# Optimization experiments

Hardware: AMD Instinct MI355X
Metric: run time of the kernel (lower is better)

## Reference

```python
import jax, jax.numpy as jnp
import numpy as np

EPS = 1e-5
C = 64  # in_channels == feat_channels == out_channels


def _ln(x, g, b):
    m = jnp.mean(x, axis=-1, keepdims=True)
    v = jnp.mean(jnp.square(x - m), axis=-1, keepdims=True)
    return (x - m) * jax.lax.rsqrt(v + EPS) * g + b


def setup_inputs() -> dict:
    key = jax.random.key(0)
    ks = jax.random.split(key, 10)
    bs, nc, H, W = 8, 80, 256, 256
    d = {
        "feat": jax.random.normal(ks[0], (bs, C, H, W), jnp.float32),
        "head": jax.random.normal(ks[1], (bs, nc, C, 1), jnp.float32),
        "pred": jax.random.normal(ks[2], (bs, nc, H // 2, W // 2), jnp.float32),
        # linear transforms (stored [in, out], applied as x @ W + b)
        "W_pred_t": jax.random.normal(ks[3], (C, 2 * C), jnp.float32) * 0.05,
        "b_pred_t": jnp.zeros((2 * C,), jnp.float32),
        "W_head_t": jax.random.normal(ks[4], (C, 2 * C), jnp.float32) * 0.05,
        "b_head_t": jnp.zeros((2 * C,), jnp.float32),
        "W_pred_g": jax.random.normal(ks[5], (C, C), jnp.float32) * 0.05,
        "b_pred_g": jnp.zeros((C,), jnp.float32),
        "W_head_g": jax.random.normal(ks[6], (C, C), jnp.float32) * 0.05,
        "b_head_g": jnp.zeros((C,), jnp.float32),
        "W_fc": jax.random.normal(ks[7], (C, C), jnp.float32) * 0.05,
        "b_fc": jnp.zeros((C,), jnp.float32),
        # layernorm params
        "g_pin": jnp.ones((C,), jnp.float32), "be_pin": jnp.zeros((C,), jnp.float32),
        "g_hin": jnp.ones((C,), jnp.float32), "be_hin": jnp.zeros((C,), jnp.float32),
        "g_pout": jnp.ones((C,), jnp.float32), "be_pout": jnp.zeros((C,), jnp.float32),
        "g_hout": jnp.ones((C,), jnp.float32), "be_hout": jnp.zeros((C,), jnp.float32),
        "g_fc": jnp.ones((C,), jnp.float32), "be_fc": jnp.zeros((C,), jnp.float32),
    }
    return d


def reference(feat, head, pred,
              W_pred_t, b_pred_t, W_head_t, b_head_t,
              W_pred_g, b_pred_g, W_head_g, b_head_g,
              W_fc, b_fc,
              g_pin, be_pin, g_hin, be_hin,
              g_pout, be_pout, g_hout, be_hout,
              g_fc, be_fc):
    bs, nc = head.shape[:2]
    H, W = feat.shape[2], feat.shape[3]
    pred_up = jax.image.resize(pred, (bs, nc, H, W), method="bilinear")
    pred_up = jax.nn.sigmoid(pred_up)
    # head-aware feature assembly: [bs, nc, C]
    assemble = jnp.einsum("bnhw,bchw->bnc", pred_up, feat)
    a = assemble.reshape(-1, C)                      # [BN, C]
    BN = a.shape[0]
    # head: [bs, nc, C, kk] -> [BN, kk, C]
    hd = jnp.transpose(head.reshape(bs, nc, C, -1), (0, 1, 3, 2)).reshape(BN, -1, C)

    pf = a @ W_pred_t + b_pred_t                     # [BN, 2C]
    pf_in, pf_out = pf[:, :C], pf[:, C:]
    hf = hd @ W_head_t + b_head_t                    # [BN, kk, 2C]
    hf_in, hf_out = hf[..., :C], hf[..., C:]

    gate = hf_in * pf_in[:, None, :]                 # [BN, kk, C]
    head_gate = jax.nn.sigmoid(_ln(gate @ W_head_g + b_head_g, g_hin, be_hin))
    pred_gate = jax.nn.sigmoid(_ln(gate @ W_pred_g + b_pred_g, g_pin, be_pin))

    hf_out = _ln(hf_out, g_hout, be_hout)
    pf_out = _ln(pf_out, g_pout, be_pout)

    upd = pred_gate * pf_out[:, None, :] + head_gate * hf_out
    upd = jax.nn.relu(_ln(upd @ W_fc + b_fc, g_fc, be_fc))
    upd = upd.reshape(bs, nc, -1, C)
    upd = jnp.transpose(upd, (0, 1, 3, 2)).reshape(bs, nc, C, 1, 1)
    return upd
```

## Files before the change

### kernel.cpp

```cpp
#include <hip/hip_runtime.h>
#include <hip/hip_bf16.h>
#include <hip/hip_fp16.h>


using bf16x8 = __attribute__((ext_vector_type(8))) short;
using f32x4  = __attribute__((ext_vector_type(4))) float;

#define SCHED_FENCE() __builtin_amdgcn_sched_barrier(0)
#define LGKM_BARRIER() do { \
  asm volatile("s_waitcnt lgkmcnt(0)" ::: "memory"); \
  __builtin_amdgcn_s_barrier(); } while (0)
#define GLD4(dst, ptr) \
  asm volatile("global_load_dwordx4 %0, %1, off" : "=v"(dst) : "v"(ptr) : "memory")
#define GLD1(dst, ptr) \
  asm volatile("global_load_dword %0, %1, off" : "=v"(dst) : "v"(ptr) : "memory")
#define WAITV(n) do { \
  asm volatile("s_waitcnt vmcnt(" #n ")" ::: "memory"); \
  __builtin_amdgcn_sched_barrier(0); } while (0)

__device__ __forceinline__ unsigned pk2(float lo, float hi) {
  union { __hip_bfloat162 h2; unsigned u; } cv;
  cv.h2 = __float22bfloat162_rn(make_float2(lo, hi));
  return cv.u;
}
__device__ __forceinline__ float sigAB(float a, float b) {
  return __builtin_amdgcn_rcpf(1.0f + __builtin_amdgcn_exp2f(-0.36067376f * a - 1.08202128f * b));
}
__device__ __forceinline__ float sigBA(float a, float b) {
  return __builtin_amdgcn_rcpf(1.0f + __builtin_amdgcn_exp2f(-1.08202128f * a - 0.36067376f * b));
}

__global__ __launch_bounds__(256, 3) void k_assemble_half(
    const float* __restrict__ feat, const float* __restrict__ pred,
    __half* __restrict__ partial) {
  __shared__ __align__(16) unsigned short Pfrag[20 * 64 * 8];

  const int bid = blockIdx.x;
  const int wg  = (bid & 7) * 512 + (bid >> 3);
  const int half = wg & 1;
  const int h    = (wg >> 1) & 255;
  const int b    = wg >> 9;

  const int tid = threadIdx.x;
  const int gg = tid & 15, nbp = tid >> 4;
  const int wid = tid >> 6, l = tid & 63;
  const int ch16 = l & 15, kg = l >> 4, c0 = wid << 4;

  const int j = h >> 1;
  int r0, r1; float wy0, wy1;
  if ((h & 1) == 0) { r0 = (j > 0) ? j - 1 : 0; r1 = j; wy0 = 0.25f; wy1 = 0.75f; }
  else              { r0 = j; r1 = (j < 127) ? j + 1 : 127; wy0 = 0.75f; wy1 = 0.25f; }

  const int cbase = half << 6;
  const int csc   = 64 - half;
  const float* pbat = pred + (((size_t)(b * 80)) << 14);

  f32x4 p0[5], p1[5];
  float s0[5], s1[5];
  f32x4 f[8];
  #pragma unroll
  for (int i = 0; i < 5; ++i) {
    const float* pb = pbat + (((size_t)(nbp + 16 * i)) << 14);
    GLD4(p0[i], pb + (r0 << 7) + cbase + 4 * gg);
    GLD4(p1[i], pb + (r1 << 7) + cbase + 4 * gg);
  }
  #pragma unroll
  for (int i = 0; i < 5; ++i) {
    const float* pb = pbat + (((size_t)(nbp + 16 * i)) << 14);
    GLD1(s0[i], pb + (r0 << 7) + csc);
    GLD1(s1[i], pb + (r1 << 7) + csc);
  }
  const float* fb = feat + (((size_t)(b * 64 + c0 + ch16)) << 16) + h * 256 + (half << 7);
  #pragma unroll
  for (int ks = 0; ks < 4; ++ks) {
    GLD4(f[2 * ks],     fb + ks * 32 + kg * 8);
    GLD4(f[2 * ks + 1], fb + ks * 32 + kg * 8 + 4);
  }

  WAITV(8);

  #pragma unroll
  for (int i = 0; i < 5; ++i) {
    const float sc = wy0 * s0[i] + wy1 * s1[i];
    const float y0 = wy0 * p0[i][0] + wy1 * p1[i][0];
    const float y1 = wy0 * p0[i][1] + wy1 * p1[i][1];
    const float y2 = wy0 * p0[i][2] + wy1 * p1[i][2];
    const float y3 = wy0 * p0[i][3] + wy1 * p1[i][3];
    float yl = __shfl_up(y3, 1, 16);
    float yr = __shfl_down(y0, 1, 16);
    if (gg == 0)  yl = half ? sc : y0;
    if (gg == 15) yr = half ? y3 : sc;
    float P[8];
    P[0] = sigAB(yl, y0); P[1] = sigBA(y0, y1);
    P[2] = sigAB(y0, y1); P[3] = sigBA(y1, y2);
    P[4] = sigAB(y1, y2); P[5] = sigBA(y2, y3);
    P[6] = sigAB(y2, y3); P[7] = sigBA(y3, yr);
    uint4 s;
    s.x = pk2(P[0], P[1]); s.y = pk2(P[2], P[3]);
    s.z = pk2(P[4], P[5]); s.w = pk2(P[6], P[7]);
    const int ks = gg >> 2, kgw = gg & 3;
    const int slot = kgw * 16 + ((nbp ^ ks ^ (kgw << 1)) & 15);
    *(uint4*)&Pfrag[(((ks * 5 + i) * 64) + slot) * 8] = s;
  }
  LGKM_BARRIER();

  f32x4 acc[5] = {};
  #pragma unroll
  for (int ks = 0; ks < 4; ++ks) {
    if (ks == 0)      WAITV(6);
    else if (ks == 1) WAITV(4);
    else if (ks == 2) WAITV(2);
    else              WAITV(0);
    const f32x4 f0 = f[2 * ks], f1 = f[2 * ks + 1];
    union { uint4 u; bf16x8 v; } bu;
    bu.u.x = pk2(f0[0], f0[1]); bu.u.y = pk2(f0[2], f0[3]);
    bu.u.z = pk2(f1[0], f1[1]); bu.u.w = pk2(f1[2], f1[3]);
    const int slot = kg * 16 + ((ch16 ^ ks ^ (kg << 1)) & 15);
    #pragma unroll
    for (int m = 0; m < 5; ++m) {
      const bf16x8 af = *(const bf16x8*)&Pfrag[(((ks * 5 + m) * 64) + slot) * 8];
      acc[m] = __builtin_amdgcn_mfma_f32_16x16x32_bf16(af, bu.v, acc[m], 0, 0, 0);
    }
  }

  __half* po = partial + ((size_t)(b * 512 + h * 2 + half)) * (80 * 64);
  #pragma unroll
  for (int m = 0; m < 5; ++m) {
    #pragma unroll
    for (int q = 0; q < 4; ++q) {
      const int n = m * 16 + kg * 4 + q;
      po[n * 64 + c0 + ch16] = __float2half(acc[m][q]);
    }
  }
}

__global__ __launch_bounds__(256) void k_assemble_full(
    const float* __restrict__ feat, const float* __restrict__ pred,
    __half* __restrict__ partial) {
  __shared__ __align__(16) unsigned short Pfrag[40 * 64 * 8];

  const int tid = threadIdx.x;
  const int b  = blockIdx.x >> 7;
  const int rb = blockIdx.x & 127;
  const int wid = tid >> 6, l = tid & 63;
  const int ch16 = l & 15, kg = l >> 4;
  const int c0 = wid << 4;
  const int h0 = rb * 2;
  const int gg = tid & 31, nb = tid >> 5;

  f32x4 acc[5] = {};
  const float* fwave = feat + (((size_t)(b * 64 + c0 + ch16)) << 16);
  const float* pbat  = pred + (((size_t)(b * 80)) << 14);

  #pragma unroll
  for (int r = 0; r < 2; ++r) {
    const int h = h0 + r;
    const int j = h >> 1;
    int r0, r1; float wy0, wy1;
    if ((h & 1) == 0) { r0 = (j > 0) ? j - 1 : 0; r1 = j; wy0 = 0.25f; wy1 = 0.75f; }
    else              { r0 = j; r1 = (j < 127) ? j + 1 : 127; wy0 = 0.75f; wy1 = 0.25f; }

    float4 p0[10], p1[10];
    #pragma unroll
    for (int i = 0; i < 10; ++i) {
      const float* pb = pbat + (((size_t)(nb + 8 * i)) << 14);
      p0[i] = *(const float4*)(pb + (r0 << 7) + gg * 4);
      p1[i] = *(const float4*)(pb + (r1 << 7) + gg * 4);
    }
    SCHED_FENCE();

    const float* fb = fwave + h * 256;
    float4 f[16];
    #pragma unroll
    for (int ks = 0; ks < 8; ++ks) {
      const int pw = ks * 32 + kg * 8;
      f[2 * ks]     = *(const float4*)(fb + pw);
      f[2 * ks + 1] = *(const float4*)(fb + pw + 4);
    }
    SCHED_FENCE();

    #pragma unroll
    for (int i = 0; i < 10; ++i) {
      const int n = nb + 8 * i;
      const float y0 = wy0 * p0[i].x + wy1 * p1[i].x;
      const float y1 = wy0 * p0[i].y + wy1 * p1[i].y;
      const float y2 = wy0 * p0[i].z + wy1 * p1[i].z;
      const float y3 = wy0 * p0[i].w + wy1 * p1[i].w;
      float yl = __shfl_up(y3, 1, 64);   if (gg == 0)  yl = y0;
      float yr = __shfl_down(y0, 1, 64); if (gg == 31) yr = y3;
      float P[8];
      P[0] = sigAB(yl, y0); P[1] = sigBA(y0, y1);
      P[2] = sigAB(y0, y1); P[3] = sigBA(y1, y2);
      P[4] = sigAB(y1, y2); P[5] = sigBA(y2, y3);
      P[6] = sigAB(y2, y3); P[7] = sigBA(y3, yr);
      uint4 s;
      s.x = pk2(P[0], P[1]); s.y = pk2(P[2], P[3]);
      s.z = pk2(P[4], P[5]); s.w = pk2(P[6], P[7]);
      const int ks = gg >> 2, kgw = gg & 3;
      const int slot = kgw * 16 + (((n & 15) ^ ks ^ (kgw << 1)) & 15);
      *(uint4*)&Pfrag[(((ks * 5 + (n >> 4)) * 64) + slot) * 8] = s;
    }
    LGKM_BARRIER();

    #pragma unroll
    for (int ks = 0; ks < 8; ++ks) {
      const float4 f0 = f[2 * ks], f1 = f[2 * ks + 1];
      union { uint4 u; bf16x8 v; } bu;
      bu.u.x = pk2(f0.x, f0.y); bu.u.y = pk2(f0.z, f0.w);
      bu.u.z = pk2(f1.x, f1.y); bu.u.w = pk2(f1.z, f1.w);
      const int slot = kg * 16 + ((ch16 ^ ks ^ (kg << 1)) & 15);
      #pragma unroll
      for (int m = 0; m < 5; ++m) {
        const bf16x8 af = *(const bf16x8*)&Pfrag[(((ks * 5 + m) * 64) + slot) * 8];
        acc[m] = __builtin_amdgcn_mfma_f32_16x16x32_bf16(af, bu.v, acc[m], 0, 0, 0);
      }
    }
    LGKM_BARRIER();
  }

  __half* po = partial + ((size_t)(b * 128 + rb)) * (80 * 64);
  #pragma unroll
  for (int m = 0; m < 5; ++m) {
    #pragma unroll
    for (int q = 0; q < 4; ++q) {
      const int n = m * 16 + kg * 4 + q;
      po[n * 64 + c0 + ch16] = __float2half(acc[m][q]);
    }
  }
}

__device__ __forceinline__ float wred64(float v) {
  #pragma unroll
  for (int off = 32; off > 0; off >>= 1) v += __shfl_xor(v, off, 64);
  return v;
}
__device__ __forceinline__ float lnorm(float x, const float* __restrict__ g,
                                       const float* __restrict__ be, int l) {
  const float m = wred64(x) * 0.015625f;
  const float d = x - m;
  const float var = wred64(d * d) * 0.015625f;
  return d * rsqrtf(var + 1e-5f) * g[l] + be[l];
}
__device__ __forceinline__ float sigmf(float x) {
  return __builtin_amdgcn_rcpf(1.0f + __builtin_amdgcn_exp2f(-1.44269504f * x));
}

__global__ __launch_bounds__(256) void k_head(
    const __half* __restrict__ partial, const float* __restrict__ head,
    const float* __restrict__ Wpt, const float* __restrict__ bpt,
    const float* __restrict__ Wht, const float* __restrict__ bht,
    const float* __restrict__ Wpg, const float* __restrict__ bpg,
    const float* __restrict__ Whg, const float* __restrict__ bhg,
    const float* __restrict__ Wfc, const float* __restrict__ bfc,
    const float* __restrict__ g_pin, const float* __restrict__ be_pin,
    const float* __restrict__ g_hin, const float* __restrict__ be_hin,
    const float* __restrict__ g_pout, const float* __restrict__ be_pout,
    const float* __restrict__ g_hout, const float* __restrict__ be_hout,
    const float* __restrict__ g_fc, const float* __restrict__ be_fc,
    float* __restrict__ out, int npart) {
  __shared__ float red[4][64];
  __shared__ float buf[4][64];
  const int tid = threadIdx.x, c = tid & 63, q = tid >> 6;
  const int r = blockIdx.x;
  const int b = r / 80, n = r % 80;
  const int npq = npart >> 2;

  const __half* pp = partial + ((size_t)b * npart + (size_t)q * npq) * 5120 + n * 64 + c;
  float s = 0.f;
  #pragma unroll 8
  for (int jj = 0; jj < npq; ++jj) s += __half2float(pp[(size_t)jj * 5120]);
  red[q][c] = s;
  __syncthreads();

  if (q == 0) {
    const float a_c = red[0][c] + red[1][c] + red[2][c] + red[3][c];
    buf[0][c] = a_c;
    buf[1][c] = head[(size_t)r * 64 + c];

    float pf_in = bpt[c], pf_out = bpt[64 + c];
    float hf_in = bht[c], hf_out = bht[64 + c];
    #pragma unroll 8
    for (int k = 0; k < 64; ++k) {
      const float av = buf[0][k];
      const float hv = buf[1][k];
      pf_in  += av * Wpt[k * 128 + c];
      pf_out += av * Wpt[k * 128 + 64 + c];
      hf_in  += hv * Wht[k * 128 + c];
      hf_out += hv * Wht[k * 128 + 64 + c];
    }
    buf[2][c] = hf_in * pf_in;

    float hg = bhg[c], pg = bpg[c];
    #pragma unroll 8
    for (int k = 0; k < 64; ++k) {
      const float gv = buf[2][k];
      hg += gv * Whg[k * 64 + c];
      pg += gv * Wpg[k * 64 + c];
    }
    const float head_gate = sigmf(lnorm(hg, g_hin, be_hin, c));
    const float pred_gate = sigmf(lnorm(pg, g_pin, be_pin, c));
    const float hfo = lnorm(hf_out, g_hout, be_hout, c);
    const float pfo = lnorm(pf_out, g_pout, be_pout, c);
    buf[3][c] = pred_gate * pfo + head_gate * hfo;

    float fc = bfc[c];
    #pragma unroll 8
    for (int k = 0; k < 64; ++k)
      fc += buf[3][k] * Wfc[k * 64 + c];
    float o = lnorm(fc, g_fc, be_fc, c);
    out[(size_t)r * 64 + c] = fmaxf(o, 0.f);
  }
}

extern "C" void kernel_launch(void* const* d_in, const int* in_sizes, int n_in,
                              void* d_out, int out_size, void* d_ws, size_t ws_size,
                              hipStream_t stream) {
  const float* feat   = (const float*)d_in[0];
  const float* head   = (const float*)d_in[1];
  const float* pred   = (const float*)d_in[2];
  const float* Wpt    = (const float*)d_in[3];
  const float* bpt    = (const float*)d_in[4];
  const float* Wht    = (const float*)d_in[5];
  const float* bht    = (const float*)d_in[6];
  const float* Wpg    = (const float*)d_in[7];
  const float* bpg    = (const float*)d_in[8];
  const float* Whg    = (const float*)d_in[9];
  const float* bhg    = (const float*)d_in[10];
  const float* Wfc    = (const float*)d_in[11];
  const float* bfc    = (const float*)d_in[12];
  const float* g_pin  = (const float*)d_in[13];
  const float* be_pin = (const float*)d_in[14];
  const float* g_hin  = (const float*)d_in[15];
  const float* be_hin = (const float*)d_in[16];
  const float* g_pout = (const float*)d_in[17];
  const float* be_pout= (const float*)d_in[18];
  const float* g_hout = (const float*)d_in[19];
  const float* be_hout= (const float*)d_in[20];
  const float* g_fc   = (const float*)d_in[21];
  const float* be_fc  = (const float*)d_in[22];
  float* out = (float*)d_out;
  __half* partial = (__half*)d_ws;

  const bool big = ws_size >= (size_t)8 * 512 * 5120 * 2;
  const int npart = big ? 512 : 128;

  if (big)
    hipLaunchKernelGGL(k_assemble_half, dim3(4096), dim3(256), 0, stream,
                       feat, pred, partial);
  else
    hipLaunchKernelGGL(k_assemble_full, dim3(1024), dim3(256), 0, stream,
                       feat, pred, partial);

  hipLaunchKernelGGL(k_head, dim3(640), dim3(256), 0, stream,
                     partial, head, Wpt, bpt, Wht, bht, Wpg, bpg, Whg, bhg,
                     Wfc, bfc, g_pin, be_pin, g_hin, be_hin, g_pout, be_pout,
                     g_hout, be_hout, g_fc, be_fc, out, npart);
}
```

Measured before the change: 61.28 us.

## Load feat tiles directly into LDS via global_load_lds instead of registers

```diff
diff --git a/kernel.cpp b/kernel.cpp
--- a/kernel.cpp
+++ b/kernel.cpp
@@ -10,13 +10,6 @@
 #define LGKM_BARRIER() do { \
   asm volatile("s_waitcnt lgkmcnt(0)" ::: "memory"); \
   __builtin_amdgcn_s_barrier(); } while (0)
-#define GLD4(dst, ptr) \
-  asm volatile("global_load_dwordx4 %0, %1, off" : "=v"(dst) : "v"(ptr) : "memory")
-#define GLD1(dst, ptr) \
-  asm volatile("global_load_dword %0, %1, off" : "=v"(dst) : "v"(ptr) : "memory")
-#define WAITV(n) do { \
-  asm volatile("s_waitcnt vmcnt(" #n ")" ::: "memory"); \
-  __builtin_amdgcn_sched_barrier(0); } while (0)
 
 __device__ __forceinline__ unsigned pk2(float lo, float hi) {
   union { __hip_bfloat162 h2; unsigned u; } cv;
@@ -30,9 +23,10 @@
   return __builtin_amdgcn_rcpf(1.0f + __builtin_amdgcn_exp2f(-1.08202128f * a - 0.36067376f * b));
 }
 
-__global__ __launch_bounds__(256, 3) void k_assemble_half(
+__global__ __launch_bounds__(256) void k_assemble_half(
     const float* __restrict__ feat, const float* __restrict__ pred,
     __half* __restrict__ partial) {
+  __shared__ __align__(16) float FeatLds[4][2048];
   __shared__ __align__(16) unsigned short Pfrag[20 * 64 * 8];
 
   const int bid = blockIdx.x;
@@ -57,27 +51,31 @@
 
   f32x4 p0[5], p1[5];
   float s0[5], s1[5];
-  f32x4 f[8];
   #pragma unroll
   for (int i = 0; i < 5; ++i) {
     const float* pb = pbat + (((size_t)(nbp + 16 * i)) << 14);
-    GLD4(p0[i], pb + (r0 << 7) + cbase + 4 * gg);
-    GLD4(p1[i], pb + (r1 << 7) + cbase + 4 * gg);
-  }
-  #pragma unroll
-  for (int i = 0; i < 5; ++i) {
-    const float* pb = pbat + (((size_t)(nbp + 16 * i)) << 14);
-    GLD1(s0[i], pb + (r0 << 7) + csc);
-    GLD1(s1[i], pb + (r1 << 7) + csc);
-  }
-  const float* fb = feat + (((size_t)(b * 64 + c0 + ch16)) << 16) + h * 256 + (half << 7);
-  #pragma unroll
-  for (int ks = 0; ks < 4; ++ks) {
-    GLD4(f[2 * ks],     fb + ks * 32 + kg * 8);
-    GLD4(f[2 * ks + 1], fb + ks * 32 + kg * 8 + 4);
-  }
-
-  WAITV(8);
+    p0[i] = *(const f32x4*)(pb + (r0 << 7) + cbase + 4 * gg);
+    p1[i] = *(const f32x4*)(pb + (r1 << 7) + cbase + 4 * gg);
+    s0[i] = pb[(r0 << 7) + csc];
+    s1[i] = pb[(r1 << 7) + csc];
+  }
+  SCHED_FENCE();
+
+  {
+    const float* fbase = feat + (((size_t)(b * 64 + c0)) << 16) + h * 256 + (half << 7);
+    const int kg_r = l >> 4, y = l & 15;
+    #pragma unroll
+    for (int i = 0; i < 8; ++i) {
+      const int ks = i >> 1, h2 = i & 1;
+      const int ch_r = (y ^ ks ^ (kg_r << 1)) & 15;
+      const float* src = fbase + (((size_t)ch_r) << 16) + ks * 32 + kg_r * 8 + h2 * 4;
+      __builtin_amdgcn_global_load_lds(
+          (const __attribute__((address_space(1))) void*)src,
+          (__attribute__((address_space(3))) void*)((char*)&FeatLds[wid][0] + i * 1024),
+          16, 0, 0);
+    }
+  }
+  SCHED_FENCE();
 
   #pragma unroll
   for (int i = 0; i < 5; ++i) {
@@ -102,20 +100,18 @@
     const int slot = kgw * 16 + ((nbp ^ ks ^ (kgw << 1)) & 15);
     *(uint4*)&Pfrag[(((ks * 5 + i) * 64) + slot) * 8] = s;
   }
-  LGKM_BARRIER();
+  __syncthreads();
 
   f32x4 acc[5] = {};
+  const char* fw = (const char*)&FeatLds[wid][0];
   #pragma unroll
   for (int ks = 0; ks < 4; ++ks) {
-    if (ks == 0)      WAITV(6);
-    else if (ks == 1) WAITV(4);
-    else if (ks == 2) WAITV(2);
-    else              WAITV(0);
-    const f32x4 f0 = f[2 * ks], f1 = f[2 * ks + 1];
+    const int slot = kg * 16 + ((ch16 ^ ks ^ (kg << 1)) & 15);
+    const f32x4 f0 = *(const f32x4*)(fw + ks * 2048 + slot * 16);
+    const f32x4 f1 = *(const f32x4*)(fw + ks * 2048 + 1024 + slot * 16);
     union { uint4 u; bf16x8 v; } bu;
     bu.u.x = pk2(f0[0], f0[1]); bu.u.y = pk2(f0[2], f0[3]);
     bu.u.z = pk2(f1[0], f1[1]); bu.u.w = pk2(f1[2], f1[3]);
-    const int slot = kg * 16 + ((ch16 ^ ks ^ (kg << 1)) & 15);
     #pragma unroll
     for (int m = 0; m < 5; ++m) {
       const bf16x8 af = *(const bf16x8*)&Pfrag[(((ks * 5 + m) * 64) + slot) * 8];
```

After: 61.75 us. Within noise of the previous version (+0.8%).
